# Kernel optimization log

Hardware: AMD Instinct MI355X
Metric: run time of the kernel (lower is better)

Reference implementation:

```python
import jax, jax.numpy as jnp
import numpy as np

K = 3          # number of nearest neighbors (init kwarg k)
EPS = 1e-16    # PyG knn_interpolate clamps squared distance at 1e-16


def setup_inputs() -> dict:
    key = jax.random.key(0)
    ks = jax.random.split(key, 8)
    N, M, C_IN, C_SKIP, H = 4096, 16384, 256, 128, 256
    x = jax.random.normal(ks[0], (N, C_IN), dtype=jnp.float32)
    pos = jax.random.normal(ks[1], (N, 3), dtype=jnp.float32)
    x_skip = jax.random.normal(ks[2], (M, C_SKIP), dtype=jnp.float32)
    pos_skip = jax.random.normal(ks[3], (M, 3), dtype=jnp.float32)
    W1 = jax.random.normal(ks[4], (C_IN + C_SKIP, H), dtype=jnp.float32) * (1.0 / np.sqrt(C_IN + C_SKIP))
    b1 = jnp.zeros((H,), dtype=jnp.float32)
    W2 = jax.random.normal(ks[5], (H, H), dtype=jnp.float32) * (1.0 / np.sqrt(H))
    b2 = jnp.zeros((H,), dtype=jnp.float32)
    return {"x": x, "pos": pos, "x_skip": x_skip, "pos_skip": pos_skip,
            "W1": W1, "b1": b1, "W2": W2, "b2": b2}


def knn_interpolate(x, pos, pos_skip):
    # squared pairwise distances [M, N]
    d2 = (jnp.sum(pos_skip * pos_skip, -1, keepdims=True)
          - 2.0 * pos_skip @ pos.T
          + jnp.sum(pos * pos, -1))
    neg_d, idx = jax.lax.top_k(-d2, K)          # k smallest distances
    w = 1.0 / jnp.maximum(-neg_d, EPS)           # [M, K] inverse-distance weights
    feats = x[idx]                               # [M, K, C] gather
    return jnp.einsum('mk,mkc->mc', w, feats) / jnp.sum(w, -1, keepdims=True)


def reference(x, pos, x_skip, pos_skip, W1, b1, W2, b2):
    y = knn_interpolate(x, pos, pos_skip)                # [M, C_in]
    h = jnp.concatenate([y, x_skip], axis=-1)            # [M, C_in + C_skip]
    h = jax.nn.relu(h @ W1 + b1)
    return h @ W2 + b2                                    # [M, H]
```

## Files before the change

kernel.cpp:

```cpp
#include <hip/hip_runtime.h>
#include <hip/hip_bf16.h>

#define N_PTS 4096
#define M_PTS 16384
#define CIN   256
#define CSK   128
#define KDIM  384
#define HDIM  256
#define NSHARD 32
#define SHPTS (N_PTS / NSHARD)

typedef unsigned int  u32;
typedef unsigned short u16;
typedef __attribute__((ext_vector_type(8))) short bf16x8;
typedef __attribute__((ext_vector_type(4))) float f32x4;

__device__ __forceinline__ u16 f2bf(float f) {
    union { float f; u32 i; } w; w.f = f;
    u32 x = w.i;
    u32 r = x + 0x7fffu + ((x >> 16) & 1u);
    return (u16)(r >> 16);
}

__device__ __forceinline__ bool ltk(float s, int p, float t, int i) {
    return (s < t) || (s == t && p < i);
}
__device__ __forceinline__ void ins3(float s, int p,
                                     float& t0, float& t1, float& t2,
                                     int& i0, int& i1, int& i2) {
    if (ltk(s, p, t2, i2)) {
        if (ltk(s, p, t1, i1)) {
            t2 = t1; i2 = i1;
            if (ltk(s, p, t0, i0)) { t1 = t0; i1 = i0; t0 = s; i0 = p; }
            else                   { t1 = s;  i1 = p; }
        } else { t2 = s; i2 = p; }
    }
}

#define INS3BL(s, p, t0, t1, t2, i0, i1, i2)                              \
    {                                                                     \
        float _o0 = t0, _o1 = t1, _o2 = t2;                               \
        int _a0 = i0, _a1 = i1, _a2 = i2;                                 \
        bool _c0 = (s) < _o0, _c1 = (s) < _o1, _c2 = (s) < _o2;           \
        t0 = _c0 ? (s) : _o0;              i0 = _c0 ? (p) : _a0;          \
        t1 = _c0 ? _o0 : (_c1 ? (s) : _o1); i1 = _c0 ? _a0 : (_c1 ? (p) : _a1); \
        t2 = _c1 ? _o1 : (_c2 ? (s) : _o2); i2 = _c1 ? _a1 : (_c2 ? (p) : _a2); \
    }

#define INS3MM(s, p, t0, t1, t2, i0, i1, i2)                              \
    {                                                                     \
        bool _c0 = (s) < t0, _c1 = (s) < t1, _c2 = (s) < t2;              \
        int _oi0 = i0, _oi1 = i1;                                         \
        i0 = _c0 ? (p) : i0;                                              \
        i1 = _c0 ? _oi0 : (_c1 ? (p) : i1);                               \
        i2 = _c1 ? _oi1 : (_c2 ? (p) : i2);                               \
        float _ot0 = t0, _ot1 = t1;                                       \
        t0 = fminf(t0, (s));                                              \
        t1 = __builtin_amdgcn_fmed3f(_ot0, t1, (s));                      \
        t2 = __builtin_amdgcn_fmed3f(_ot1, t2, (s));                      \
    }

__global__ __launch_bounds__(256) void scanM_gemmZ(
    const float* __restrict__ pos,
    const float* __restrict__ pos_skip,
    float* __restrict__ candM,
    const float* __restrict__ x,
    const float* __restrict__ W1,
    float* __restrict__ Z)
{
    const int bid = blockIdx.x;
    const int tid = threadIdx.x;

    if (bid < 512) {
        __shared__ float4 spts[SHPTS];
        const int bx = bid & 15, sh = bid >> 4;
        const int pbase = sh * SHPTS;

        if (tid < SHPTS) {
            const int i = pbase + tid;
            float px = pos[3 * i], py = pos[3 * i + 1], pz = pos[3 * i + 2];
            float pn = __fadd_rn(__fadd_rn(__fmul_rn(px, px), __fmul_rn(py, py)),
                                 __fmul_rn(pz, pz));
            spts[tid] = make_float4(px, py, pz, pn);
        }

        const int mb = bx * 1024 + tid;
        float qx[4], qy[4], qz[4], qn[4];
        #pragma unroll
        for (int q = 0; q < 4; ++q) {
            const int m = mb + q * 256;
            qx[q] = pos_skip[3 * m];
            qy[q] = pos_skip[3 * m + 1];
            qz[q] = pos_skip[3 * m + 2];
            qn[q] = __fadd_rn(__fadd_rn(__fmul_rn(qx[q], qx[q]), __fmul_rn(qy[q], qy[q])),
                              __fmul_rn(qz[q], qz[q]));
        }
        __syncthreads();

        float e[4] = {3.4e38f, 3.4e38f, 3.4e38f, 3.4e38f};

        #pragma unroll 8
        for (int j = 0; j < SHPTS; ++j) {
            float4 v = spts[j];
            #pragma unroll
            for (int q = 0; q < 4; ++q) {
                float b = __fmaf_rn(qz[q], v.z, __fmaf_rn(qy[q], v.y, __fmul_rn(qx[q], v.x)));
                float s = __fadd_rn(__fmaf_rn(-2.0f, b, qn[q]), v.w);
                e[q] = fminf(e[q], s);
            }
        }

        #pragma unroll
        for (int q = 0; q < 4; ++q)
            candM[(size_t)sh * M_PTS + mb + q * 256] = e[q];
    } else {
        __shared__ alignas(16) u16 Bs[64][40];
        const int id = bid - 512;
        const int w = tid >> 6, l = tid & 63;
        const int bm = (id & 31) * 128;
        const int bn = (id >> 5) * 64;
        const int lr = l & 15, lg = l >> 4;

        f32x4 acc[2][4];
        #pragma unroll
        for (int mt = 0; mt < 2; ++mt)
            #pragma unroll
            for (int nt = 0; nt < 4; ++nt)
                acc[mt][nt] = (f32x4){0.f, 0.f, 0.f, 0.f};

        const int sc = tid >> 2;
        const int sk = (tid & 3) * 8;

        for (int k0 = 0; k0 < CIN; k0 += 32) {
            #pragma unroll
            for (int j = 0; j < 8; ++j)
                Bs[sc][sk + j] = f2bf(W1[(size_t)(k0 + sk + j) * HDIM + bn + sc]);
            __syncthreads();

            bf16x8 af[2];
            #pragma unroll
            for (int mt = 0; mt < 2; ++mt) {
                const float* xp = x + (size_t)(bm + w * 32 + mt * 16 + lr) * CIN + k0 + lg * 8;
                float4 h0 = *reinterpret_cast<const float4*>(xp);
                float4 h1 = *reinterpret_cast<const float4*>(xp + 4);
                af[mt][0] = (short)f2bf(h0.x); af[mt][1] = (short)f2bf(h0.y);
                af[mt][2] = (short)f2bf(h0.z); af[mt][3] = (short)f2bf(h0.w);
                af[mt][4] = (short)f2bf(h1.x); af[mt][5] = (short)f2bf(h1.y);
                af[mt][6] = (short)f2bf(h1.z); af[mt][7] = (short)f2bf(h1.w);
            }
            #pragma unroll
            for (int nt = 0; nt < 4; ++nt) {
                bf16x8 bf = *reinterpret_cast<const bf16x8*>(&Bs[nt * 16 + lr][lg * 8]);
                #pragma unroll
                for (int mt = 0; mt < 2; ++mt)
                    acc[mt][nt] = __builtin_amdgcn_mfma_f32_16x16x32_bf16(
                        af[mt], bf, acc[mt][nt], 0, 0, 0);
            }
            __syncthreads();
        }

        #pragma unroll
        for (int nt = 0; nt < 4; ++nt) {
            const int col = bn + nt * 16 + lr;
            #pragma unroll
            for (int mt = 0; mt < 2; ++mt)
                #pragma unroll
                for (int i = 0; i < 4; ++i) {
                    const int row = bm + w * 32 + mt * 16 + lg * 4 + i;
                    Z[(size_t)row * HDIM + col] = acc[mt][nt][i];
                }
        }
    }
}

__global__ __launch_bounds__(256) void knn_select_rescan(
    const float* __restrict__ pos,
    const float* __restrict__ pos_skip,
    const float* __restrict__ candM,
    float4* __restrict__ nbrw, uint4* __restrict__ nbri)
{
    __shared__ float sv[64][4][3];
    __shared__ int   si[64][4][3];
    __shared__ u32   ssel[64];
    const int tid  = threadIdx.x;
    const int ql   = tid >> 2;
    const int slot = tid & 3;
    const int m = blockIdx.x * 64 + ql;

    {
        float t0 = 3.4e38f, t1 = 3.4e38f, t2 = 3.4e38f;
        int   s0 = 63, s1 = 63, s2 = 63;
        #pragma unroll
        for (int k = 0; k < 8; ++k) {
            const int sh = slot * 8 + k;
            float mn = candM[(size_t)sh * M_PTS + m];
            INS3BL(mn, sh, t0, t1, t2, s0, s1, s2);
        }
        sv[ql][slot][0] = t0; sv[ql][slot][1] = t1; sv[ql][slot][2] = t2;
        si[ql][slot][0] = s0; si[ql][slot][1] = s1; si[ql][slot][2] = s2;
    }
    __syncthreads();
    if (slot == 0) {
        float t0 = 3.4e38f, t1 = 3.4e38f, t2 = 3.4e38f;
        int   s0 = 63, s1 = 63, s2 = 63;
        #pragma unroll
        for (int s = 0; s < 4; ++s)
            #pragma unroll
            for (int k = 0; k < 3; ++k)
                ins3(sv[ql][s][k], si[ql][s][k], t0, t1, t2, s0, s1, s2);
        ssel[ql] = (u32)s0 | ((u32)s1 << 8) | ((u32)s2 << 16);
    }
    __syncthreads();
    const u32 sel = ssel[ql];

    if (slot < 3) {
        const int sh = (sel >> (8 * slot)) & 63;
        const int pb = sh * SHPTS;

        const float qx = pos_skip[3 * m];
        const float qy = pos_skip[3 * m + 1];
        const float qz = pos_skip[3 * m + 2];
        const float qn = __fadd_rn(__fadd_rn(__fmul_rn(qx, qx), __fmul_rn(qy, qy)),
                                   __fmul_rn(qz, qz));

        float t0 = 3.4e38f, t1 = 3.4e38f, t2 = 3.4e38f;
        int   i0 = 0x7fffffff, i1 = 0x7fffffff, i2 = 0x7fffffff;

        #pragma unroll 4
        for (int j = 0; j < SHPTS; ++j) {
            const int p = pb + j;
            float px = pos[3 * p], py = pos[3 * p + 1], pz = pos[3 * p + 2];
            float pn = __fadd_rn(__fadd_rn(__fmul_rn(px, px), __fmul_rn(py, py)),
                                 __fmul_rn(pz, pz));
            float b = __fmaf_rn(qz, pz, __fmaf_rn(qy, py, __fmul_rn(qx, px)));
            float s = __fadd_rn(__fmaf_rn(-2.0f, b, qn), pn);
            INS3MM(s, p, t0, t1, t2, i0, i1, i2);
        }
        sv[ql][slot][0] = t0; sv[ql][slot][1] = t1; sv[ql][slot][2] = t2;
        si[ql][slot][0] = i0; si[ql][slot][1] = i1; si[ql][slot][2] = i2;
    }
    __syncthreads();

    if (slot == 0) {
        float t0 = 3.4e38f, t1 = 3.4e38f, t2 = 3.4e38f;
        int   i0 = 0x7fffffff, i1 = 0x7fffffff, i2 = 0x7fffffff;
        #pragma unroll
        for (int s = 0; s < 3; ++s)
            #pragma unroll
            for (int k = 0; k < 3; ++k)
                ins3(sv[ql][s][k], si[ql][s][k], t0, t1, t2, i0, i1, i2);

        float w0 = __fdiv_rn(1.0f, fmaxf(t0, 1e-16f));
        float w1 = __fdiv_rn(1.0f, fmaxf(t1, 1e-16f));
        float w2 = __fdiv_rn(1.0f, fmaxf(t2, 1e-16f));
        float inv = __fdiv_rn(1.0f, __fadd_rn(__fadd_rn(w0, w1), w2));
        nbrw[m] = make_float4(w0 * inv, w1 * inv, w2 * inv, 0.f);
        nbri[m] = make_uint4((u32)i0, (u32)i1, (u32)i2, 0u);
    }
}

__global__ __launch_bounds__(256) void gemm_SH(
    const float* __restrict__ x_skip, const float* __restrict__ W1,
    const float* __restrict__ b1, const float* __restrict__ Z,
    const float4* __restrict__ nbrw, const uint4* __restrict__ nbri,
    u16* __restrict__ H)
{
    __shared__ alignas(16) u16 Bs[64][40];
    const int tid = threadIdx.x;
    const int w = tid >> 6, l = tid & 63;
    const int bm = blockIdx.x * 128;
    const int bn = blockIdx.y * 64;
    const int lr = l & 15, lg = l >> 4;

    f32x4 acc[2][4];
    #pragma unroll
    for (int mt = 0; mt < 2; ++mt)
        #pragma unroll
        for (int nt = 0; nt < 4; ++nt)
            acc[mt][nt] = (f32x4){0.f, 0.f, 0.f, 0.f};

    const int sc = tid >> 2;
    const int sk = (tid & 3) * 8;

    for (int k0 = 0; k0 < CSK; k0 += 32) {
        #pragma unroll
        for (int j = 0; j < 8; ++j)
            Bs[sc][sk + j] = f2bf(W1[(size_t)(CIN + k0 + sk + j) * HDIM + bn + sc]);
        __syncthreads();

        bf16x8 af[2];
        #pragma unroll
        for (int mt = 0; mt < 2; ++mt) {
            const float* xp = x_skip + (size_t)(bm + w * 32 + mt * 16 + lr) * CSK + k0 + lg * 8;
            float4 h0 = *reinterpret_cast<const float4*>(xp);
            float4 h1 = *reinterpret_cast<const float4*>(xp + 4);
            af[mt][0] = (short)f2bf(h0.x); af[mt][1] = (short)f2bf(h0.y);
            af[mt][2] = (short)f2bf(h0.z); af[mt][3] = (short)f2bf(h0.w);
            af[mt][4] = (short)f2bf(h1.x); af[mt][5] = (short)f2bf(h1.y);
            af[mt][6] = (short)f2bf(h1.z); af[mt][7] = (short)f2bf(h1.w);
        }
        #pragma unroll
        for (int nt = 0; nt < 4; ++nt) {
            bf16x8 bf = *reinterpret_cast<const bf16x8*>(&Bs[nt * 16 + lr][lg * 8]);
            #pragma unroll
            for (int mt = 0; mt < 2; ++mt)
                acc[mt][nt] = __builtin_amdgcn_mfma_f32_16x16x32_bf16(
                    af[mt], bf, acc[mt][nt], 0, 0, 0);
        }
        __syncthreads();
    }

    #pragma unroll
    for (int mt = 0; mt < 2; ++mt) {
        #pragma unroll
        for (int i = 0; i < 4; ++i) {
            const int row = bm + w * 32 + mt * 16 + lg * 4 + i;
            const float4 wv = nbrw[row];
            const uint4  iv = nbri[row];
            const float* z0 = Z + (size_t)(iv.x & 4095u) * HDIM;
            const float* z1 = Z + (size_t)(iv.y & 4095u) * HDIM;
            const float* z2 = Z + (size_t)(iv.z & 4095u) * HDIM;
            #pragma unroll
            for (int nt = 0; nt < 4; ++nt) {
                const int col = bn + nt * 16 + lr;
                float zb = wv.x * z0[col] + wv.y * z1[col] + wv.z * z2[col];
                float v = acc[mt][nt][i] + zb + b1[col];
                H[(size_t)row * HDIM + col] = f2bf(v > 0.f ? v : 0.f);
            }
        }
    }
}

__global__ __launch_bounds__(256) void gemm2_mfma(
    const u16* __restrict__ H, const float* __restrict__ W2,
    const float* __restrict__ b2, float* __restrict__ out)
{
    __shared__ alignas(16) u16 Bs[64][40];
    const int tid = threadIdx.x;
    const int w = tid >> 6, l = tid & 63;
    const int bm = blockIdx.x * 128;
    const int bn = blockIdx.y * 64;
    const int lr = l & 15, lg = l >> 4;

    f32x4 acc[2][4];
    #pragma unroll
    for (int mt = 0; mt < 2; ++mt)
        #pragma unroll
        for (int nt = 0; nt < 4; ++nt)
            acc[mt][nt] = (f32x4){0.f, 0.f, 0.f, 0.f};

    const int sc = tid >> 2;
    const int sk = (tid & 3) * 8;

    for (int k0 = 0; k0 < HDIM; k0 += 32) {
        #pragma unroll
        for (int j = 0; j < 8; ++j)
            Bs[sc][sk + j] = f2bf(W2[(size_t)(k0 + sk + j) * HDIM + bn + sc]);
        __syncthreads();

        bf16x8 af[2];
        #pragma unroll
        for (int mt = 0; mt < 2; ++mt) {
            const int row = bm + w * 32 + mt * 16 + lr;
            af[mt] = *reinterpret_cast<const bf16x8*>(H + (size_t)row * HDIM + k0 + lg * 8);
        }
        #pragma unroll
        for (int nt = 0; nt < 4; ++nt) {
            bf16x8 bf = *reinterpret_cast<const bf16x8*>(&Bs[nt * 16 + lr][lg * 8]);
            #pragma unroll
            for (int mt = 0; mt < 2; ++mt)
                acc[mt][nt] = __builtin_amdgcn_mfma_f32_16x16x32_bf16(
                    af[mt], bf, acc[mt][nt], 0, 0, 0);
        }
        __syncthreads();
    }

    #pragma unroll
    for (int nt = 0; nt < 4; ++nt) {
        const int col = bn + nt * 16 + lr;
        const float bias = b2[col];
        #pragma unroll
        for (int mt = 0; mt < 2; ++mt)
            #pragma unroll
            for (int i = 0; i < 4; ++i) {
                const int row = bm + w * 32 + mt * 16 + lg * 4 + i;
                out[(size_t)row * HDIM + col] = acc[mt][nt][i] + bias;
            }
    }
}

extern "C" void kernel_launch(void* const* d_in, const int* in_sizes, int n_in,
                              void* d_out, int out_size, void* d_ws, size_t ws_size,
                              hipStream_t stream) {
    const float* x        = (const float*)d_in[0];
    const float* pos      = (const float*)d_in[1];
    const float* x_skip   = (const float*)d_in[2];
    const float* pos_skip = (const float*)d_in[3];
    const float* W1       = (const float*)d_in[4];
    const float* b1       = (const float*)d_in[5];
    const float* W2       = (const float*)d_in[6];
    const float* b2       = (const float*)d_in[7];

    u16*    Hbuf = (u16*)d_ws;
    float*  Z    = (float*)((char*)d_ws + (8u << 20));
    float4* nbrw = (float4*)((char*)d_ws + (12u << 20));
    uint4*  nbri = (uint4*)((char*)d_ws + (12u << 20) + (256u << 10));

    float* candM = (float*)d_out;
    float* out   = (float*)d_out;

    scanM_gemmZ      <<<640, 256, 0, stream>>>(pos, pos_skip, candM, x, W1, Z);
    knn_select_rescan<<<256, 256, 0, stream>>>(pos, pos_skip, candM, nbrw, nbri);
    gemm_SH          <<<dim3(128, 4), 256, 0, stream>>>(x_skip, W1, b1, Z, nbrw, nbri, Hbuf);
    gemm2_mfma       <<<dim3(128, 4), 256, 0, stream>>>(Hbuf, W2, b2, out);
}
```

Measured before the change: 64.07 us.

## Fuse first and second MLP GEMMs into one kernel via shared-memory H tile

Merges the skip-GEMM/ReLU kernel and the second GEMM into a single kernel in which each block computes a 64-row tile across all 256 hidden columns. The tile is kept in LDS as bf16 and fed straight into the W2 GEMM. This removes the global H round trip and one kernel launch. In exchange the grid shrinks to 256 blocks, each thread holds 16 accumulators, LDS use grows to roughly 54KB, and the blocks redundantly convert all of W1 and W2 to bf16, which may hurt occupancy.

Measured after the change: 77.34 us. +20.7%, slower.

```diff
diff --git a/kernel.cpp b/kernel.cpp
--- a/kernel.cpp
+++ b/kernel.cpp
@@ -259,133 +259,110 @@
     }
 }
 
-__global__ __launch_bounds__(256) void gemm_SH(
+__global__ __launch_bounds__(256) void gemm_SH2(
     const float* __restrict__ x_skip, const float* __restrict__ W1,
     const float* __restrict__ b1, const float* __restrict__ Z,
     const float4* __restrict__ nbrw, const uint4* __restrict__ nbri,
-    u16* __restrict__ H)
+    const float* __restrict__ W2, const float* __restrict__ b2,
+    float* __restrict__ out)
 {
-    __shared__ alignas(16) u16 Bs[64][40];
+    __shared__ alignas(16) u16 Bs[256][40];
+    __shared__ alignas(16) u16 Hs[64][264];
     const int tid = threadIdx.x;
     const int w = tid >> 6, l = tid & 63;
-    const int bm = blockIdx.x * 128;
-    const int bn = blockIdx.y * 64;
+    const int bm = blockIdx.x * 64;
     const int lr = l & 15, lg = l >> 4;
-
-    f32x4 acc[2][4];
-    #pragma unroll
-    for (int mt = 0; mt < 2; ++mt)
-        #pragma unroll
-        for (int nt = 0; nt < 4; ++nt)
-            acc[mt][nt] = (f32x4){0.f, 0.f, 0.f, 0.f};
 
     const int sc = tid >> 2;
     const int sk = (tid & 3) * 8;
 
-    for (int k0 = 0; k0 < CSK; k0 += 32) {
-        #pragma unroll
-        for (int j = 0; j < 8; ++j)
-            Bs[sc][sk + j] = f2bf(W1[(size_t)(CIN + k0 + sk + j) * HDIM + bn + sc]);
-        __syncthreads();
-
-        bf16x8 af[2];
-        #pragma unroll
-        for (int mt = 0; mt < 2; ++mt) {
-            const float* xp = x_skip + (size_t)(bm + w * 32 + mt * 16 + lr) * CSK + k0 + lg * 8;
+    {
+        f32x4 acc[16];
+        #pragma unroll
+        for (int nt = 0; nt < 16; ++nt) acc[nt] = (f32x4){0.f, 0.f, 0.f, 0.f};
+
+        for (int k0 = 0; k0 < CSK; k0 += 32) {
+            #pragma unroll
+            for (int cc = 0; cc < 4; ++cc) {
+                const int c = cc * 64 + sc;
+                #pragma unroll
+                for (int j = 0; j < 8; ++j)
+                    Bs[c][sk + j] = f2bf(W1[(size_t)(CIN + k0 + sk + j) * HDIM + c]);
+            }
+            __syncthreads();
+
+            const float* xp = x_skip + (size_t)(bm + w * 16 + lr) * CSK + k0 + lg * 8;
             float4 h0 = *reinterpret_cast<const float4*>(xp);
             float4 h1 = *reinterpret_cast<const float4*>(xp + 4);
-            af[mt][0] = (short)f2bf(h0.x); af[mt][1] = (short)f2bf(h0.y);
-            af[mt][2] = (short)f2bf(h0.z); af[mt][3] = (short)f2bf(h0.w);
-            af[mt][4] = (short)f2bf(h1.x); af[mt][5] = (short)f2bf(h1.y);
-            af[mt][6] = (short)f2bf(h1.z); af[mt][7] = (short)f2bf(h1.w);
-        }
-        #pragma unroll
-        for (int nt = 0; nt < 4; ++nt) {
-            bf16x8 bf = *reinterpret_cast<const bf16x8*>(&Bs[nt * 16 + lr][lg * 8]);
-            #pragma unroll
-            for (int mt = 0; mt < 2; ++mt)
-                acc[mt][nt] = __builtin_amdgcn_mfma_f32_16x16x32_bf16(
-                    af[mt], bf, acc[mt][nt], 0, 0, 0);
-        }
-        __syncthreads();
-    }
-
-    #pragma unroll
-    for (int mt = 0; mt < 2; ++mt) {
+            bf16x8 af;
+            af[0] = (short)f2bf(h0.x); af[1] = (short)f2bf(h0.y);
+            af[2] = (short)f2bf(h0.z); af[3] = (short)f2bf(h0.w);
+            af[4] = (short)f2bf(h1.x); af[5] = (short)f2bf(h1.y);
+            af[6] = (short)f2bf(h1.z); af[7] = (short)f2bf(h1.w);
+
+            #pragma unroll
+            for (int nt = 0; nt < 16; ++nt) {
+                bf16x8 bf = *reinterpret_cast<const bf16x8*>(&Bs[nt * 16 + lr][lg * 8]);
+                acc[nt] = __builtin_amdgcn_mfma_f32_16x16x32_bf16(af, bf, acc[nt], 0, 0, 0);
+            }
+            __syncthreads();
+        }
+
         #pragma unroll
         for (int i = 0; i < 4; ++i) {
-            const int row = bm + w * 32 + mt * 16 + lg * 4 + i;
+            const int lrow = w * 16 + lg * 4 + i;
+            const int row  = bm + lrow;
             const float4 wv = nbrw[row];
             const uint4  iv = nbri[row];
             const float* z0 = Z + (size_t)(iv.x & 4095u) * HDIM;
             const float* z1 = Z + (size_t)(iv.y & 4095u) * HDIM;
             const float* z2 = Z + (size_t)(iv.z & 4095u) * HDIM;
             #pragma unroll
-            for (int nt = 0; nt < 4; ++nt) {
-                const int col = bn + nt * 16 + lr;
+            for (int nt = 0; nt < 16; ++nt) {
+                const int col = nt * 16 + lr;
                 float zb = wv.x * z0[col] + wv.y * z1[col] + wv.z * z2[col];
-                float v = acc[mt][nt][i] + zb + b1[col];
-                H[(size_t)row * HDIM + col] = f2bf(v > 0.f ? v : 0.f);
-            }
-        }
-    }
-}
-
-__global__ __launch_bounds__(256) void gemm2_mfma(
-    const u16* __restrict__ H, const float* __restrict__ W2,
-    const float* __restrict__ b2, float* __restrict__ out)
-{
-    __shared__ alignas(16) u16 Bs[64][40];
-    const int tid = threadIdx.x;
-    const int w = tid >> 6, l = tid & 63;
-    const int bm = blockIdx.x * 128;
-    const int bn = blockIdx.y * 64;
-    const int lr = l & 15, lg = l >> 4;
-
-    f32x4 acc[2][4];
-    #pragma unroll
-    for (int mt = 0; mt < 2; ++mt)
-        #pragma unroll
-        for (int nt = 0; nt < 4; ++nt)
-            acc[mt][nt] = (f32x4){0.f, 0.f, 0.f, 0.f};
-
-    const int sc = tid >> 2;
-    const int sk = (tid & 3) * 8;
-
-    for (int k0 = 0; k0 < HDIM; k0 += 32) {
-        #pragma unroll
-        for (int j = 0; j < 8; ++j)
-            Bs[sc][sk + j] = f2bf(W2[(size_t)(k0 + sk + j) * HDIM + bn + sc]);
-        __syncthreads();
-
-        bf16x8 af[2];
-        #pragma unroll
-        for (int mt = 0; mt < 2; ++mt) {
-            const int row = bm + w * 32 + mt * 16 + lr;
-            af[mt] = *reinterpret_cast<const bf16x8*>(H + (size_t)row * HDIM + k0 + lg * 8);
-        }
-        #pragma unroll
-        for (int nt = 0; nt < 4; ++nt) {
-            bf16x8 bf = *reinterpret_cast<const bf16x8*>(&Bs[nt * 16 + lr][lg * 8]);
-            #pragma unroll
-            for (int mt = 0; mt < 2; ++mt)
-                acc[mt][nt] = __builtin_amdgcn_mfma_f32_16x16x32_bf16(
-                    af[mt], bf, acc[mt][nt], 0, 0, 0);
-        }
-        __syncthreads();
-    }
-
-    #pragma unroll
-    for (int nt = 0; nt < 4; ++nt) {
-        const int col = bn + nt * 16 + lr;
-        const float bias = b2[col];
-        #pragma unroll
-        for (int mt = 0; mt < 2; ++mt)
+                float v = acc[nt][i] + zb + b1[col];
+                Hs[lrow][col] = f2bf(v > 0.f ? v : 0.f);
+            }
+        }
+    }
+    __syncthreads();
+
+    {
+        f32x4 acc[16];
+        #pragma unroll
+        for (int nt = 0; nt < 16; ++nt) acc[nt] = (f32x4){0.f, 0.f, 0.f, 0.f};
+
+        for (int k0 = 0; k0 < HDIM; k0 += 32) {
+            #pragma unroll
+            for (int cc = 0; cc < 4; ++cc) {
+                const int c = cc * 64 + sc;
+                #pragma unroll
+                for (int j = 0; j < 8; ++j)
+                    Bs[c][sk + j] = f2bf(W2[(size_t)(k0 + sk + j) * HDIM + c]);
+            }
+            __syncthreads();
+
+            bf16x8 af = *reinterpret_cast<const bf16x8*>(&Hs[w * 16 + lr][k0 + lg * 8]);
+
+            #pragma unroll
+            for (int nt = 0; nt < 16; ++nt) {
+                bf16x8 bf = *reinterpret_cast<const bf16x8*>(&Bs[nt * 16 + lr][lg * 8]);
+                acc[nt] = __builtin_amdgcn_mfma_f32_16x16x32_bf16(af, bf, acc[nt], 0, 0, 0);
+            }
+            __syncthreads();
+        }
+
+        #pragma unroll
+        for (int nt = 0; nt < 16; ++nt) {
+            const int col = nt * 16 + lr;
+            const float bias = b2[col];
             #pragma unroll
             for (int i = 0; i < 4; ++i) {
-                const int row = bm + w * 32 + mt * 16 + lg * 4 + i;
-                out[(size_t)row * HDIM + col] = acc[mt][nt][i] + bias;
-            }
+                const int row = bm + w * 16 + lg * 4 + i;
+                out[(size_t)row * HDIM + col] = acc[nt][i] + bias;
+            }
+        }
     }
 }
 
@@ -401,16 +378,14 @@
     const float* W2       = (const float*)d_in[6];
     const float* b2       = (const float*)d_in[7];
 
-    u16*    Hbuf = (u16*)d_ws;
-    float*  Z    = (float*)((char*)d_ws + (8u << 20));
-    float4* nbrw = (float4*)((char*)d_ws + (12u << 20));
-    uint4*  nbri = (uint4*)((char*)d_ws + (12u << 20) + (256u << 10));
+    float*  Z    = (float*)d_ws;
+    float4* nbrw = (float4*)((char*)d_ws + (4u << 20));
+    uint4*  nbri = (uint4*)((char*)d_ws + (4u << 20) + (256u << 10));
 
     float* candM = (float*)d_out;
     float* out   = (float*)d_out;
 
     scanM_gemmZ      <<<640, 256, 0, stream>>>(pos, pos_skip, candM, x, W1, Z);
     knn_select_rescan<<<256, 256, 0, stream>>>(pos, pos_skip, candM, nbrw, nbri);
-    gemm_SH          <<<dim3(128, 4), 256, 0, stream>>>(x_skip, W1, b1, Z, nbrw, nbri, Hbuf);
-    gemm2_mfma       <<<dim3(128, 4), 256, 0, stream>>>(Hbuf, W2, b2, out);
-}
+    gemm_SH2         <<<256, 256, 0, stream>>>(x_skip, W1, b1, Z, nbrw, nbri, W2, b2, out);
+}
```
